# Performance work log

Measured on AMD Instinct MI355X. Metric: run time of the kernel, lower is better.

Reference implementation:

```python
import jax, jax.numpy as jnp
import numpy as np

H = 128  # hidden size


def setup_inputs() -> dict:
    key = jax.random.key(0)
    ks = jax.random.split(key, 16)
    B, N, L = 32, 64, 256
    s_in = 1.0  # fan-in 1 for layer-0 input weights
    s_h = 1.0 / np.sqrt(H)
    u = lambda k, shape, s: jax.random.uniform(k, shape, jnp.float32, -s, s)
    return {
        "x": jax.random.normal(ks[0], (B, N, L), jnp.float32),
        # LSTM layer 0 (input_size=1), PyTorch gate order i,f,g,o
        "W_ih0": u(ks[1], (4 * H, 1), s_h),
        "W_hh0": u(ks[2], (4 * H, H), s_h),
        "b_ih0": u(ks[3], (4 * H,), s_h),
        "b_hh0": u(ks[4], (4 * H,), s_h),
        # LSTM layer 1 (input_size=H)
        "W_ih1": u(ks[5], (4 * H, H), s_h),
        "W_hh1": u(ks[6], (4 * H, H), s_h),
        "b_ih1": u(ks[7], (4 * H,), s_h),
        "b_hh1": u(ks[8], (4 * H,), s_h),
        # MLP head: Linear(H,H) -> ReLU -> Linear(H,1)
        "W1": u(ks[9], (H, H), s_h),
        "b1": u(ks[10], (H,), s_h),
        "W2": u(ks[11], (1, H), s_h),
        "b2": u(ks[12], (1,), s_h),
        "asset_bias": jnp.zeros((N,), jnp.float32),
    }


def _lstm_cell(x_t, h, c, W_ih, W_hh, b_ih, b_hh):
    g = x_t @ W_ih.T + b_ih + h @ W_hh.T + b_hh  # [BN, 4H]
    i, f, gg, o = jnp.split(g, 4, axis=-1)
    c = jax.nn.sigmoid(f) * c + jax.nn.sigmoid(i) * jnp.tanh(gg)
    h = jax.nn.sigmoid(o) * jnp.tanh(c)
    return h, c


def reference(x, W_ih0, W_hh0, b_ih0, b_hh0, W_ih1, W_hh1, b_ih1, b_hh1,
              W1, b1, W2, b2, asset_bias):
    B, N, L = x.shape
    BN = B * N
    # [L, BN, 1] time-major input (input_size = 1)
    xs = jnp.swapaxes(x.reshape(BN, L), 0, 1)[:, :, None]

    def step(carry, x_t):
        h1, c1, h2, c2 = carry
        h1, c1 = _lstm_cell(x_t, h1, c1, W_ih0, W_hh0, b_ih0, b_hh0)
        h2, c2 = _lstm_cell(h1, h2, c2, W_ih1, W_hh1, b_ih1, b_hh1)
        return (h1, c1, h2, c2), None

    z = jnp.zeros((BN, H), x.dtype)
    (h1, c1, h2, c2), _ = jax.lax.scan(step, (z, z, z, z), xs)
    h_last = h2  # last timestep output of top layer (dropout inactive in eval)
    s = jax.nn.relu(h_last @ W1.T + b1) @ W2.T + b2  # [BN, 1]
    s = s.reshape(B, N) + asset_bias
    return jax.nn.softmax(s, axis=1)
```

## Files before the change

### kernel.cpp

```cpp
#include <hip/hip_runtime.h>

#define H 128
#define L 256
#define SB 8
#define NBLK 256
#define NTHR 512

typedef _Float16 f16x8 __attribute__((ext_vector_type(8)));
typedef float f32x4 __attribute__((ext_vector_type(4)));

#define MFMA(accv, av, bv) accv = __builtin_amdgcn_mfma_f32_16x16x32_f16(av, bv, accv, 0, 0, 0)

__device__ __forceinline__ float fsig(float x) {
  return __builtin_amdgcn_rcpf(1.f + __builtin_amdgcn_exp2f(-1.44269504089f * x));
}
__device__ __forceinline__ float ftanh(float x) {
  return 2.f * __builtin_amdgcn_rcpf(1.f + __builtin_amdgcn_exp2f(-2.88539008178f * x)) - 1.f;
}


__global__ __launch_bounds__(NTHR, 2) void lstm_kernel(
    const float* __restrict__ xg,
    const float* __restrict__ Wih0, const float* __restrict__ Whh0,
    const float* __restrict__ bih0, const float* __restrict__ bhh0,
    const float* __restrict__ Wih1, const float* __restrict__ Whh1,
    const float* __restrict__ bih1, const float* __restrict__ bhh1,
    const float* __restrict__ W1,   const float* __restrict__ b1v,
    const float* __restrict__ W2,   const float* __restrict__ b2v,
    const float* __restrict__ abias,
    float* __restrict__ out_scores)
{
  __shared__ __align__(16) _Float16 Whh1_s[512 * H];
  __shared__ __align__(16) float    x_s[L * SB];
  __shared__ __align__(16) _Float16 h1_s[2][16 * H];
  __shared__ __align__(16) _Float16 h2_s[2][16 * H];

  const int tid  = threadIdx.x;
  const int lane = tid & 63;
  const int w    = tid >> 6;
  const int l15  = lane & 15;
  const int lhi  = lane >> 4;
  const int sb   = blockIdx.x * SB;

  for (int i = tid; i < SB * L; i += NTHR) {
    int s = i >> 8, t = i & 255;
    x_s[t * SB + s] = xg[(sb + s) * L + t];
  }
  for (int i = tid; i < 512 * H; i += NTHR) {
    int r = i >> 7, k = i & 127;
    Whh1_s[(r << 7) + (k ^ ((r & 7) << 3))] = (_Float16)Whh1[i];
  }
  for (int i = tid; i < 16 * H; i += NTHR) {
    h1_s[0][i] = (_Float16)0.f; h1_s[1][i] = (_Float16)0.f;
    h2_s[0][i] = (_Float16)0.f; h2_s[1][i] = (_Float16)0.f;
  }

  f16x8 whh0f[4][4], wih1f[4][4];
  float b0r[4], b1r[4], w0r[4];
  #pragma unroll
  for (int n = 0; n < 4; ++n) {
    const int c = (n << 7) + (w << 4) + l15;
    b0r[n] = bih0[c] + bhh0[c];
    b1r[n] = bih1[c] + bhh1[c];
    w0r[n] = Wih0[c];
    #pragma unroll
    for (int kk = 0; kk < 4; ++kk) {
      const float* p0 = Whh0 + c * H + (kk << 5) + (lhi << 3);
      const float* p1 = Wih1 + c * H + (kk << 5) + (lhi << 3);
      f16x8 f0, f1;
      #pragma unroll
      for (int j = 0; j < 8; ++j) { f0[j] = (_Float16)p0[j]; f1[j] = (_Float16)p1[j]; }
      whh0f[n][kk] = f0; wih1f[n][kk] = f1;
    }
  }

  float c1[2] = {0.f, 0.f}, c2[2] = {0.f, 0.f};
  const int colh  = (w << 4) | l15;
  const int rown0 = lhi << 2;
  const int so0   = lhi << 1;
  const int arow  = l15 << 7;
  const int aswz  = (l15 & 7) << 3;
  int wrow[4];
  #pragma unroll
  for (int n = 0; n < 4; ++n) wrow[n] = ((n << 7) + colh) << 7;

  __syncthreads();

  #pragma unroll 1
  for (int t = 0; t <= L; ++t) {
    const int pw = t & 1;
    const int pr = pw ^ 1;

    f16x8 a1f[4], a2f[4];
    #pragma unroll
    for (int kk = 0; kk < 4; ++kk) {
      const int kb = (kk << 5) + (lhi << 3);
      a1f[kk] = *(const f16x8*)&h1_s[pr][arow + (kb ^ aswz)];
      a2f[kk] = *(const f16x8*)&h2_s[pw][arow + (kb ^ aswz)];
    }
    f16x8 whh1t[4][4];
    #pragma unroll
    for (int kk = 0; kk < 4; ++kk) {
      const int kb = (kk << 5) + (lhi << 3);
      #pragma unroll
      for (int n = 0; n < 4; ++n)
        whh1t[kk][n] = *(const f16x8*)&Whh1_s[wrow[n] + (kb ^ aswz)];
    }

    f32x4 acc0[4], acc1[4];
    #pragma unroll
    for (int n = 0; n < 4; ++n) {
      acc0[n] = (f32x4){0.f, 0.f, 0.f, 0.f};
      acc1[n] = (f32x4){0.f, 0.f, 0.f, 0.f};
    }

    #pragma unroll
    for (int kk = 0; kk < 4; ++kk) {
      MFMA(acc0[0], a1f[kk], whh0f[0][kk]);
      MFMA(acc0[1], a1f[kk], whh0f[1][kk]);
      MFMA(acc0[2], a1f[kk], whh0f[2][kk]);
      MFMA(acc0[3], a1f[kk], whh0f[3][kk]);
      MFMA(acc1[0], a1f[kk], wih1f[0][kk]);
      MFMA(acc1[1], a1f[kk], wih1f[1][kk]);
      MFMA(acc1[2], a1f[kk], wih1f[2][kk]);
      MFMA(acc1[3], a1f[kk], wih1f[3][kk]);
    }
    #pragma unroll
    for (int kk = 0; kk < 4; ++kk) {
      MFMA(acc1[0], a2f[kk], whh1t[kk][0]);
      MFMA(acc1[1], a2f[kk], whh1t[kk][1]);
      MFMA(acc1[2], a2f[kk], whh1t[kk][2]);
      MFMA(acc1[3], a2f[kk], whh1t[kk][3]);
    }

    if (t < L) {
      const float2 xv = *(const float2*)&x_s[t * SB + so0];
      float h1n[2];
      #pragma unroll
      for (int r = 0; r < 2; ++r) {
        const float x0 = r ? xv.y : xv.x;
        float ig = fsig (acc0[0][r] + x0 * w0r[0] + b0r[0]);
        float fg = fsig (acc0[1][r] + x0 * w0r[1] + b0r[1]);
        float gg = ftanh(acc0[2][r] + x0 * w0r[2] + b0r[2]);
        float og = fsig (acc0[3][r] + x0 * w0r[3] + b0r[3]);
        float c = fg * c1[r] + ig * gg;
        c1[r] = c;
        h1n[r] = og * ftanh(c);
      }
      #pragma unroll
      for (int r = 0; r < 2; ++r) {
        const int row = rown0 + r;
        h1_s[pw][(row << 7) + (colh ^ ((row & 7) << 3))] = (_Float16)h1n[r];
      }
    }
    if (t > 0) {
      float h2n[2];
      #pragma unroll
      for (int r = 0; r < 2; ++r) {
        float ig = fsig (acc1[0][r] + b1r[0]);
        float fg = fsig (acc1[1][r] + b1r[1]);
        float gg = ftanh(acc1[2][r] + b1r[2]);
        float og = fsig (acc1[3][r] + b1r[3]);
        float c = fg * c2[r] + ig * gg;
        c2[r] = c;
        h2n[r] = og * ftanh(c);
      }
      #pragma unroll
      for (int r = 0; r < 2; ++r) {
        const int row = rown0 + r;
        h2_s[pr][(row << 7) + (colh ^ ((row & 7) << 3))] = (_Float16)h2n[r];
      }
    }
    __syncthreads();
  }

  float* W1t = (float*)Whh1_s;
  for (int i = tid; i < H * H; i += NTHR) {
    int j = i >> 7, k = i & 127;
    W1t[(k << 7) + j] = W1[i];
  }
  __syncthreads();
  {
    const int s   = w;
    const int row = ((s >> 1) << 2) | (s & 1);
    float a0 = 0.f, a1 = 0.f;
    for (int k = 0; k < H; ++k) {
      float hv = (float)h2_s[1][(row << 7) + (k ^ ((row & 7) << 3))];
      a0 += hv * W1t[(k << 7) + lane];
      a1 += hv * W1t[(k << 7) + lane + 64];
    }
    a0 = fmaxf(a0 + b1v[lane], 0.f);
    a1 = fmaxf(a1 + b1v[lane + 64], 0.f);
    float part = a0 * W2[lane] + a1 * W2[lane + 64];
    #pragma unroll
    for (int off = 32; off >= 1; off >>= 1) part += __shfl_xor(part, off, 64);
    if (lane == 0)
      out_scores[sb + s] = part + b2v[0] + abias[(sb + s) & 63];
  }
}

__global__ void softmax_kernel(float* __restrict__ out) {
  const int b = blockIdx.x, n = threadIdx.x;
  float v = out[(b << 6) + n];
  float m = v;
  #pragma unroll
  for (int off = 32; off >= 1; off >>= 1) m = fmaxf(m, __shfl_xor(m, off, 64));
  float e = __builtin_amdgcn_exp2f((v - m) * 1.44269504089f);
  float s = e;
  #pragma unroll
  for (int off = 32; off >= 1; off >>= 1) s += __shfl_xor(s, off, 64);
  out[(b << 6) + n] = e / s;
}

extern "C" void kernel_launch(void* const* d_in, const int* in_sizes, int n_in,
                              void* d_out, int out_size, void* d_ws, size_t ws_size,
                              hipStream_t stream) {
  (void)in_sizes; (void)n_in; (void)d_ws; (void)ws_size; (void)out_size;
  const float* xg   = (const float*)d_in[0];
  const float* Wih0 = (const float*)d_in[1];
  const float* Whh0 = (const float*)d_in[2];
  const float* bih0 = (const float*)d_in[3];
  const float* bhh0 = (const float*)d_in[4];
  const float* Wih1 = (const float*)d_in[5];
  const float* Whh1 = (const float*)d_in[6];
  const float* bih1 = (const float*)d_in[7];
  const float* bhh1 = (const float*)d_in[8];
  const float* W1   = (const float*)d_in[9];
  const float* b1   = (const float*)d_in[10];
  const float* W2   = (const float*)d_in[11];
  const float* b2   = (const float*)d_in[12];
  const float* ab   = (const float*)d_in[13];
  float* out = (float*)d_out;

  lstm_kernel<<<NBLK, NTHR, 0, stream>>>(xg, Wih0, Whh0, bih0, bhh0,
                                         Wih1, Whh1, bih1, bhh1,
                                         W1, b1, W2, b2, ab, out);
  softmax_kernel<<<32, 64, 0, stream>>>(out);
}
```

Before: 476.5 us.

## Interleave layer-1 gate math with layer-0 MFMAs and double-buffer Whh1 fragments

Each timestep is reordered so the layer-1 MFMAs run first. Layer 1's activations and cell update then execute while layer 0's MFMAs issue, and sched_group_barrier hints interleave VALU work with MFMA. Biases and the x·W_ih0 term are folded into the accumulator initial values. The t<L and t>0 branches become branchless: the x index is clamped and a zero mask applied to c2. Whh1 LDS fragments are now loaded one k-chunk ahead into two register buffers instead of all at once. This cuts register pressure and hides LDS latency, at the cost of a rigid schedule and some redundant work on the first and last steps.

```diff
diff --git a/kernel.cpp b/kernel.cpp
--- a/kernel.cpp
+++ b/kernel.cpp
@@ -90,28 +90,79 @@
   for (int t = 0; t <= L; ++t) {
     const int pw = t & 1;
     const int pr = pw ^ 1;
-
-    f16x8 a1f[4], a2f[4];
+    const int tx = (t < L) ? t : (L - 1);
+    const float zm = (t > 0) ? 1.f : 0.f;
+
+    f16x8 a1f[4], a2f[4], wt0[4], wt1[4];
     #pragma unroll
     for (int kk = 0; kk < 4; ++kk) {
       const int kb = (kk << 5) + (lhi << 3);
       a1f[kk] = *(const f16x8*)&h1_s[pr][arow + (kb ^ aswz)];
       a2f[kk] = *(const f16x8*)&h2_s[pw][arow + (kb ^ aswz)];
     }
-    f16x8 whh1t[4][4];
-    #pragma unroll
-    for (int kk = 0; kk < 4; ++kk) {
-      const int kb = (kk << 5) + (lhi << 3);
+    {
+      const int kb = (lhi << 3);
       #pragma unroll
       for (int n = 0; n < 4; ++n)
-        whh1t[kk][n] = *(const f16x8*)&Whh1_s[wrow[n] + (kb ^ aswz)];
-    }
+        wt0[n] = *(const f16x8*)&Whh1_s[wrow[n] + (kb ^ aswz)];
+    }
+    const float2 xv = *(const float2*)&x_s[tx * SB + so0];
 
     f32x4 acc0[4], acc1[4];
     #pragma unroll
     for (int n = 0; n < 4; ++n) {
-      acc0[n] = (f32x4){0.f, 0.f, 0.f, 0.f};
-      acc1[n] = (f32x4){0.f, 0.f, 0.f, 0.f};
+      acc0[n][0] = xv.x * w0r[n] + b0r[n];
+      acc0[n][1] = xv.y * w0r[n] + b0r[n];
+      acc0[n][2] = 0.f; acc0[n][3] = 0.f;
+      acc1[n][0] = b1r[n]; acc1[n][1] = b1r[n];
+      acc1[n][2] = 0.f; acc1[n][3] = 0.f;
+    }
+    __builtin_amdgcn_sched_barrier(0);
+
+    #pragma unroll
+    for (int kk = 0; kk < 4; ++kk) {
+      MFMA(acc1[0], a1f[kk], wih1f[0][kk]);
+      MFMA(acc1[1], a1f[kk], wih1f[1][kk]);
+      MFMA(acc1[2], a1f[kk], wih1f[2][kk]);
+      MFMA(acc1[3], a1f[kk], wih1f[3][kk]);
+    }
+    #pragma unroll
+    for (int kk = 0; kk < 4; ++kk) {
+      if (kk < 3) {
+        const int kb = ((kk + 1) << 5) + (lhi << 3);
+        if ((kk & 1) == 0) {
+          #pragma unroll
+          for (int n = 0; n < 4; ++n)
+            wt1[n] = *(const f16x8*)&Whh1_s[wrow[n] + (kb ^ aswz)];
+        } else {
+          #pragma unroll
+          for (int n = 0; n < 4; ++n)
+            wt0[n] = *(const f16x8*)&Whh1_s[wrow[n] + (kb ^ aswz)];
+        }
+      }
+      if ((kk & 1) == 0) {
+        MFMA(acc1[0], a2f[kk], wt0[0]);
+        MFMA(acc1[1], a2f[kk], wt0[1]);
+        MFMA(acc1[2], a2f[kk], wt0[2]);
+        MFMA(acc1[3], a2f[kk], wt0[3]);
+      } else {
+        MFMA(acc1[0], a2f[kk], wt1[0]);
+        MFMA(acc1[1], a2f[kk], wt1[1]);
+        MFMA(acc1[2], a2f[kk], wt1[2]);
+        MFMA(acc1[3], a2f[kk], wt1[3]);
+      }
+    }
+
+    float h2n[2];
+    #pragma unroll
+    for (int r = 0; r < 2; ++r) {
+      float ig = fsig (acc1[0][r]);
+      float fg = fsig (acc1[1][r]);
+      float gg = ftanh(acc1[2][r]);
+      float og = fsig (acc1[3][r]);
+      float cn = zm * (fg * c2[r] + ig * gg);
+      c2[r] = cn;
+      h2n[r] = og * ftanh(cn);
     }
 
     #pragma unroll
@@ -120,57 +171,34 @@
       MFMA(acc0[1], a1f[kk], whh0f[1][kk]);
       MFMA(acc0[2], a1f[kk], whh0f[2][kk]);
       MFMA(acc0[3], a1f[kk], whh0f[3][kk]);
-      MFMA(acc1[0], a1f[kk], wih1f[0][kk]);
-      MFMA(acc1[1], a1f[kk], wih1f[1][kk]);
-      MFMA(acc1[2], a1f[kk], wih1f[2][kk]);
-      MFMA(acc1[3], a1f[kk], wih1f[3][kk]);
-    }
-    #pragma unroll
-    for (int kk = 0; kk < 4; ++kk) {
-      MFMA(acc1[0], a2f[kk], whh1t[kk][0]);
-      MFMA(acc1[1], a2f[kk], whh1t[kk][1]);
-      MFMA(acc1[2], a2f[kk], whh1t[kk][2]);
-      MFMA(acc1[3], a2f[kk], whh1t[kk][3]);
-    }
-
-    if (t < L) {
-      const float2 xv = *(const float2*)&x_s[t * SB + so0];
-      float h1n[2];
-      #pragma unroll
-      for (int r = 0; r < 2; ++r) {
-        const float x0 = r ? xv.y : xv.x;
-        float ig = fsig (acc0[0][r] + x0 * w0r[0] + b0r[0]);
-        float fg = fsig (acc0[1][r] + x0 * w0r[1] + b0r[1]);
-        float gg = ftanh(acc0[2][r] + x0 * w0r[2] + b0r[2]);
-        float og = fsig (acc0[3][r] + x0 * w0r[3] + b0r[3]);
-        float c = fg * c1[r] + ig * gg;
-        c1[r] = c;
-        h1n[r] = og * ftanh(c);
-      }
-      #pragma unroll
-      for (int r = 0; r < 2; ++r) {
-        const int row = rown0 + r;
-        h1_s[pw][(row << 7) + (colh ^ ((row & 7) << 3))] = (_Float16)h1n[r];
-      }
-    }
-    if (t > 0) {
-      float h2n[2];
-      #pragma unroll
-      for (int r = 0; r < 2; ++r) {
-        float ig = fsig (acc1[0][r] + b1r[0]);
-        float fg = fsig (acc1[1][r] + b1r[1]);
-        float gg = ftanh(acc1[2][r] + b1r[2]);
-        float og = fsig (acc1[3][r] + b1r[3]);
-        float c = fg * c2[r] + ig * gg;
-        c2[r] = c;
-        h2n[r] = og * ftanh(c);
-      }
-      #pragma unroll
-      for (int r = 0; r < 2; ++r) {
-        const int row = rown0 + r;
-        h2_s[pr][(row << 7) + (colh ^ ((row & 7) << 3))] = (_Float16)h2n[r];
-      }
-    }
+    }
+    float h1n[2];
+    #pragma unroll
+    for (int r = 0; r < 2; ++r) {
+      float ig = fsig (acc0[0][r]);
+      float fg = fsig (acc0[1][r]);
+      float gg = ftanh(acc0[2][r]);
+      float og = fsig (acc0[3][r]);
+      float cc = fg * c1[r] + ig * gg;
+      c1[r] = cc;
+      h1n[r] = og * ftanh(cc);
+    }
+
+    #pragma unroll
+    for (int r = 0; r < 2; ++r) {
+      const int row = rown0 + r;
+      h1_s[pw][(row << 7) + (colh ^ ((row & 7) << 3))] = (_Float16)h1n[r];
+      h2_s[pr][(row << 7) + (colh ^ ((row & 7) << 3))] = (_Float16)h2n[r];
+    }
+
+    __builtin_amdgcn_sched_group_barrier(0x008, 32, 0);
+    #pragma unroll
+    for (int i = 0; i < 8; ++i) {
+      __builtin_amdgcn_sched_group_barrier(0x008, 2, 0);
+      __builtin_amdgcn_sched_group_barrier(0x002, 7, 0);
+    }
+    __builtin_amdgcn_sched_group_barrier(0x002, 56, 0);
+    __builtin_amdgcn_sched_group_barrier(0x200, 4, 0);
     __syncthreads();
   }
 
```

After: 530.5 us. 1.11x slower.
